# Optimization experiments

Measured on AMD Instinct MI355X. Metric: run time of the kernel, lower is better.

## Reference

```python
import jax, jax.numpy as jnp
import numpy as np

B, S = 4, 4096
DIM = 256
DF = 128   # dim_fourier = floor(256*0.5)
DS = 128   # dim_spline = 256 - 128
GF = 5     # fourier grid_size
GS = 5     # spline grid_size
K = 3      # spline order
P = 0.5
MIN_FREQ = 1e-6
LN_EPS = 1e-5


def _spline_grid():
    h = 2.0 / GS  # grid_range [-1, 1]
    g = np.arange(-K, GS + K + 1, dtype=np.float32) * h - 1.0
    return jnp.asarray(np.broadcast_to(g, (DS, g.shape[0])).copy())  # (DS, GS+2K+1)


def _base_freq():
    return jnp.asarray((1.0 / 10 ** np.linspace(0, 9, DF, dtype=np.float32)).reshape(DF, 1))


def b_splines(x, grid):
    # x: (N, DS); grid: (DS, GS+2K+1). Recursive de Boor B-spline basis.
    xe = x[:, :, None]
    bases = ((xe >= grid[:, :-1]) & (xe < grid[:, 1:])).astype(x.dtype)  # (N, DS, GS+2K)
    for k in range(1, K + 1):
        left = (xe - grid[:, : -(k + 1)]) / (grid[:, k:-1] - grid[:, : -(k + 1)])
        right = (grid[:, k + 1:] - xe) / (grid[:, k + 1:] - grid[:, 1:-k])
        bases = left * bases[:, :, :-1] + right * bases[:, :, 1:]
    return bases  # (N, DS, GS+K)


def setup_inputs() -> dict:
    key = jax.random.key(0)
    ks = jax.random.split(key, 8)
    timestamps = jax.random.uniform(ks[0], (B, S), dtype=jnp.float32)
    freq_theta = jnp.zeros((DF, 1), dtype=jnp.float32)
    bias_fourier = jnp.zeros((DF,), dtype=jnp.float32)
    fourier_weight = jax.random.normal(ks[1], (2, DF, DF, GF), dtype=jnp.float32) / (
        np.sqrt(DF) * np.sqrt(GF))
    w1_spline_w = jnp.asarray((1.0 / 10 ** np.linspace(0, 9, DS, dtype=np.float32)).reshape(DS, 1))
    w1_spline_b = jnp.zeros((DS,), dtype=jnp.float32)
    base_weight = jax.random.normal(ks[2], (DS, DS), dtype=jnp.float32) / np.sqrt(DS)
    spline_weight = jax.random.normal(ks[3], (DS, DS, GS + K), dtype=jnp.float32) / np.sqrt(DS * (GS + K))
    scale_weight = jnp.ones((DIM,), dtype=jnp.float32)
    ln_weight = jnp.ones((DIM,), dtype=jnp.float32)
    ln_bias = jnp.zeros((DIM,), dtype=jnp.float32)
    return {
        "timestamps": timestamps,
        "freq_theta": freq_theta,
        "bias_fourier": bias_fourier,
        "fourier_weight": fourier_weight,
        "w1_spline_w": w1_spline_w,
        "w1_spline_b": w1_spline_b,
        "base_weight": base_weight,
        "spline_weight": spline_weight,
        "scale_weight": scale_weight,
        "ln_weight": ln_weight,
        "ln_bias": ln_bias,
    }


def reference(timestamps, freq_theta, bias_fourier, fourier_weight,
              w1_spline_w, w1_spline_b, base_weight, spline_weight,
              scale_weight, ln_weight, ln_bias):
    grid = _spline_grid()
    base_freq = _base_freq()
    t = timestamps[..., None]  # (B, S, 1)

    # ---- Fourier branch ----
    freq_scale = jax.nn.softplus(freq_theta) + MIN_FREQ          # (DF, 1)
    freq_weight = base_freq * freq_scale                          # (DF, 1)
    proj_f = t * freq_weight[:, 0] + bias_fourier                 # (B, S, DF)
    xf = proj_f.reshape(-1, DF)                                   # (N, DF)
    kfreq = jnp.arange(1, GF + 1, dtype=xf.dtype)                 # (GF,)
    arg = xf[:, :, None] * kfreq                                  # (N, DF, GF)
    # Same math as torch's broadcast-then-sum, expressed as a contraction:
    # y[n,o] = sum_{d,g} cos(arg)[n,d,g] * Wc[o,d,g] + sin * Ws
    y_f = (jnp.einsum('ndg,odg->no', jnp.cos(arg), fourier_weight[0])
           + jnp.einsum('ndg,odg->no', jnp.sin(arg), fourier_weight[1])
           + fourier_weight[0].dtype.type(0) + jnp.zeros((DF,), xf.dtype))
    y_f = y_f  # bias of FourierSeries is zeros param; include explicitly below
    fourier_bias = jnp.zeros((DF,), xf.dtype)
    y_f = y_f + fourier_bias
    out_fourier = y_f.reshape(B, S, DF)

    # ---- Spline branch ----
    proj_s = t * w1_spline_w[:, 0] + w1_spline_b                  # (B, S, DS)
    xs = proj_s.reshape(-1, DS)                                   # (N, DS)
    base_out = jnp.tanh(xs) @ base_weight.T                       # (N, DS)
    bsp = b_splines(xs, grid).reshape(xs.shape[0], -1)            # (N, DS*(GS+K))
    spline_out = bsp @ spline_weight.reshape(DS, -1).T            # (N, DS)
    out_spline = (base_out + spline_out).reshape(B, S, DS)

    # ---- Combine (padded concat == concat of weighted halves) ----
    out = jnp.concatenate([out_fourier * P, out_spline * (1.0 - P)], axis=-1)  # (B, S, DIM)

    # LayerNorm then learnable scale
    mu = jnp.mean(out, axis=-1, keepdims=True)
    var = jnp.mean((out - mu) ** 2, axis=-1, keepdims=True)
    out = (out - mu) * jax.lax.rsqrt(var + LN_EPS) * ln_weight + ln_bias
    out = out * scale_weight
    return out
```

## Files before the change

### kernel.cpp

```cpp
#include <hip/hip_runtime.h>


typedef __attribute__((ext_vector_type(8))) _Float16 half8;
typedef __attribute__((ext_vector_type(2))) __fp16 fp16x2;
typedef __attribute__((ext_vector_type(4))) float f32x4;

#define KN5 -0.19999998807907104f
#define KN6  0.20000004768371582f
#define KN7  0.60000002384185791f

__device__ __forceinline__ unsigned pk(float a, float b) {
    fp16x2 h = __builtin_amdgcn_cvt_pkrtz(a, b);
    return __builtin_bit_cast(unsigned, h);
}

#define SPL9(x, o0,o1,o2,o3,o4,o5,o6,o7,o8) do {                          \
    float ax_ = fabsf(x);                                                  \
    float e_  = __expf(-2.f*ax_);                                          \
    float th_ = (1.f - e_) * __builtin_amdgcn_rcpf(1.f + e_);              \
    o0 = ((x) < 0.f) ? -th_ : th_;                                         \
    bool b1_ = ((x) >= KN6), b2_ = ((x) >= KN7);                           \
    float kn_ = b2_ ? KN7 : (b1_ ? KN6 : KN5);                             \
    float u_  = ((x) - kn_) * 2.5f;                                        \
    float um_ = 1.f - u_;                                                  \
    float u2_ = u_*u_, u3_ = u2_*u_, um2_ = um_*um_, um3_ = um2_*um_;      \
    float w0_ = (1.f/6.f)*um3_, w3_ = (1.f/6.f)*u3_;                       \
    float w1_ = 0.6666666666666667f - u2_  + 0.5f*u3_;                     \
    float w2_ = 0.6666666666666667f - um2_ + 0.5f*um3_;                    \
    o1 = 0.f; o2 = 0.f;                                                    \
    o3 = b1_ ? 0.f : w0_;                                                  \
    o4 = b2_ ? 0.f : (b1_ ? w0_ : w1_);                                    \
    o5 = b2_ ? w0_ : (b1_ ? w1_ : w2_);                                    \
    o6 = b2_ ? w1_ : (b1_ ? w2_ : w3_);                                    \
    o7 = b2_ ? w2_ : (b1_ ? w3_ : 0.f);                                    \
    o8 = b2_ ? w3_ : 0.f;                                                  \
} while (0)

__global__ __launch_bounds__(256) void prep_kernel(
    const float* __restrict__ FW,
    const float* __restrict__ BW,
    const float* __restrict__ SW,
    _Float16* __restrict__ WFP, _Float16* __restrict__ WSP)
{
    int tt = blockIdx.x * 256 + threadIdx.x;
    if (tt < 163840) {
        float val = FW[tt];
        int g = tt % 5;
        int r1 = tt / 5;
        int d = r1 & 127;
        int r2 = r1 >> 7;
        int col = r2 & 127;
        int p = r2 >> 7;
        int k = d*10 + p*5 + g;
        int idx = (((col>>4)*40 + (k>>5))*64 + ((k>>3)&3)*16 + (col&15))*8 + (k&7);
        WFP[idx] = (_Float16)val;
    } else if (tt < 180224) {
        int s = tt - 163840;
        float val = BW[s];
        int col = s >> 7, d = s & 127;
        int k = d*9;
        int idx = (((col>>4)*36 + (k>>5))*64 + ((k>>3)&3)*16 + (col&15))*8 + (k&7);
        WSP[idx] = (_Float16)val;
    } else if (tt < 311296) {
        int s = tt - 180224;
        float val = SW[s];
        int m = s & 7, d = (s>>3) & 127, col = s >> 10;
        int k = d*9 + m + 1;
        int idx = (((col>>4)*36 + (k>>5))*64 + ((k>>3)&3)*16 + (col&15))*8 + (k&7);
        WSP[idx] = (_Float16)val;
    }
}

__global__ __launch_bounds__(512) void fused_kernel(
    const float* __restrict__ TS, const float* __restrict__ FTHETA,
    const float* __restrict__ BFOUR, const float* __restrict__ W1W,
    const float* __restrict__ W1B, const float* __restrict__ LNW,
    const float* __restrict__ LNB, const float* __restrict__ SCW,
    const _Float16* __restrict__ WFP, const _Float16* __restrict__ WSP,
    float* __restrict__ OUT)
{
    __shared__ __align__(128) _Float16 feat0[64 * 288];
    __shared__ __align__(128) _Float16 feat1[64 * 288];
    __shared__ float tsS[64], fwS[128], bfS[128], w1wS[128], w1bS[128];
    __shared__ float redS[64][4], redQ[64][4], muS[64], rsS[64];

    const int tid  = threadIdx.x;
    const int lane = tid & 63;
    const int w    = tid >> 6;
    const int wr   = w >> 2, wc = w & 3;
    const int la15 = lane & 15, lhi = lane >> 4;
    const int row0 = blockIdx.x * 64;

    if (tid < 64) tsS[tid] = TS[row0 + tid];
    else if (tid < 192) {
        int d = tid - 64;
        float th = FTHETA[d];
        float sp = (th > 20.f) ? th : log1pf(__expf(th));
        float ex = (float)((double)d * (9.0 / 127.0));
        fwS[d] = (1.0f / powf(10.f, ex)) * (sp + 1e-6f);
        bfS[d] = BFOUR[d];
    } else if (tid < 320) {
        int d = tid - 192;
        w1wS[d] = W1W[d];
        w1bS[d] = W1B[d];
    }
    __syncthreads();

    f32x4 acc1[2][2] = {};
    f32x4 acc2[2][2] = {};

    auto computeFour = [&](int ch, _Float16* buf) {
#pragma unroll
        for (int q = 0; q < 2; ++q) {
            int task = q * 512 + tid;
            int row = task >> 4, dd = task & 15;
            int d = (ch << 4) + dd;
            float base = tsS[row] * fwS[d] + bfS[d];
            float s1, c1;
            __sincosf(base, &s1, &c1);
            float tc = c1 + c1;
            float c2 = tc*c1 - 1.f, c3 = tc*c2 - c1, c4 = tc*c3 - c2, c5 = tc*c4 - c3;
            float s2 = tc*s1,       s3 = tc*s2 - s1, s4 = tc*s3 - s2, s5 = tc*s4 - s3;
            char* p = (char*)buf;
            int b = row * 576 + dd * 20;
            int sw = (row & 7) << 4;
            *(unsigned*)(p + ((b +  0) ^ sw)) = pk(c1, c2);
            *(unsigned*)(p + ((b +  4) ^ sw)) = pk(c3, c4);
            *(unsigned*)(p + ((b +  8) ^ sw)) = pk(c5, s1);
            *(unsigned*)(p + ((b + 12) ^ sw)) = pk(s2, s3);
            *(unsigned*)(p + ((b + 16) ^ sw)) = pk(s4, s5);
        }
    };

    auto computeSpl = [&](int ch, _Float16* buf) {
#pragma unroll
        for (int q = 0; q < 2; ++q) {
            int task = q * 512 + tid;
            int row = task >> 4, dp = task & 15;
            float t = tsS[row];
            int d0 = (ch << 5) + dp * 2;
            float x0 = t * w1wS[d0]     + w1bS[d0];
            float x1 = t * w1wS[d0 + 1] + w1bS[d0 + 1];
            float a0,a1,a2,a3,a4,a5,a6,a7,a8;
            float b0,b1,b2,b3,b4,b5,b6,b7,b8;
            SPL9(x0, a0,a1,a2,a3,a4,a5,a6,a7,a8);
            SPL9(x1, b0,b1,b2,b3,b4,b5,b6,b7,b8);
            char* p = (char*)buf;
            int b = row * 576 + dp * 36;
            int sw = (row & 7) << 4;
            *(unsigned*)(p + ((b +  0) ^ sw)) = pk(a0, a1);
            *(unsigned*)(p + ((b +  4) ^ sw)) = pk(a2, a3);
            *(unsigned*)(p + ((b +  8) ^ sw)) = pk(a4, a5);
            *(unsigned*)(p + ((b + 12) ^ sw)) = pk(a6, a7);
            *(unsigned*)(p + ((b + 16) ^ sw)) = pk(a8, b0);
            *(unsigned*)(p + ((b + 20) ^ sw)) = pk(b1, b2);
            *(unsigned*)(p + ((b + 24) ^ sw)) = pk(b3, b4);
            *(unsigned*)(p + ((b + 28) ^ sw)) = pk(b5, b6);
            *(unsigned*)(p + ((b + 32) ^ sw)) = pk(b7, b8);
        }
    };

    auto mfmaFour = [&](int ch, const _Float16* buf) {
        const char* p = (const char*)buf;
#pragma unroll
        for (int kt = 0; kt < 5; ++kt) {
            int ktg = ch * 5 + kt;
            half8 bf0 = *(const half8*)(WFP + (size_t)(((wc*2 + 0)*40 + ktg)*64 + lane) * 8);
            half8 bf1 = *(const half8*)(WFP + (size_t)(((wc*2 + 1)*40 + ktg)*64 + lane) * 8);
#pragma unroll
            for (int rt = 0; rt < 2; ++rt) {
                int row = wr*32 + rt*16 + la15;
                half8 a = *(const half8*)(p + ((row*576 + kt*64 + lhi*16) ^ ((row & 7) << 4)));
                acc1[rt][0] = __builtin_amdgcn_mfma_f32_16x16x32_f16(a, bf0, acc1[rt][0], 0, 0, 0);
                acc1[rt][1] = __builtin_amdgcn_mfma_f32_16x16x32_f16(a, bf1, acc1[rt][1], 0, 0, 0);
            }
        }
    };

    auto mfmaSpl = [&](int ch, const _Float16* buf) {
        const char* p = (const char*)buf;
#pragma unroll
        for (int kt = 0; kt < 9; ++kt) {
            int ktg = ch * 9 + kt;
            half8 bf0 = *(const half8*)(WSP + (size_t)(((wc*2 + 0)*36 + ktg)*64 + lane) * 8);
            half8 bf1 = *(const half8*)(WSP + (size_t)(((wc*2 + 1)*36 + ktg)*64 + lane) * 8);
#pragma unroll
            for (int rt = 0; rt < 2; ++rt) {
                int row = wr*32 + rt*16 + la15;
                half8 a = *(const half8*)(p + ((row*576 + kt*64 + lhi*16) ^ ((row & 7) << 4)));
                acc2[rt][0] = __builtin_amdgcn_mfma_f32_16x16x32_f16(a, bf0, acc2[rt][0], 0, 0, 0);
                acc2[rt][1] = __builtin_amdgcn_mfma_f32_16x16x32_f16(a, bf1, acc2[rt][1], 0, 0, 0);
            }
        }
    };

    computeFour(0, feat0);
    __syncthreads();
    for (int ph = 0; ph < 12; ++ph) {
        _Float16* nb = ((ph + 1) & 1) ? feat1 : feat0;
        const _Float16* cb = (ph & 1) ? feat1 : feat0;
        int nx = ph + 1;
        if (nx < 8)        computeFour(nx, nb);
        else if (nx < 12)  computeSpl(nx - 8, nb);
        if (ph < 8) mfmaFour(ph, cb);
        else        mfmaSpl(ph - 8, cb);
        __syncthreads();
    }

#pragma unroll
    for (int rt = 0; rt < 2; ++rt) {
#pragma unroll
        for (int j = 0; j < 4; ++j) {
            float x0 = 0.5f * acc1[rt][0][j];
            float x1 = 0.5f * acc1[rt][1][j];
            float x2 = 0.5f * acc2[rt][0][j];
            float x3 = 0.5f * acc2[rt][1][j];
            float s  = x0 + x1 + x2 + x3;
            float qq = x0*x0 + x1*x1 + x2*x2 + x3*x3;
#pragma unroll
            for (int m = 1; m < 16; m <<= 1) {
                s  += __shfl_xor(s, m);
                qq += __shfl_xor(qq, m);
            }
            if (la15 == 0) {
                int r = wr*32 + rt*16 + lhi*4 + j;
                redS[r][wc] = s;
                redQ[r][wc] = qq;
            }
        }
    }
    __syncthreads();
    if (tid < 64) {
        float s = redS[tid][0] + redS[tid][1] + redS[tid][2] + redS[tid][3];
        float qq = redQ[tid][0] + redQ[tid][1] + redQ[tid][2] + redQ[tid][3];
        float mu = s * (1.0f / 256.0f);
        float var = qq * (1.0f / 256.0f) - mu * mu;
        muS[tid] = mu;
        rsS[tid] = rsqrtf(var + 1e-5f);
    }
    __syncthreads();
    {
        int c10 = wc*32 + la15, c11 = c10 + 16;
        int c20 = c10 + 128,    c21 = c11 + 128;
        float g10 = LNW[c10]*SCW[c10], h10 = LNB[c10]*SCW[c10];
        float g11 = LNW[c11]*SCW[c11], h11 = LNB[c11]*SCW[c11];
        float g20 = LNW[c20]*SCW[c20], h20 = LNB[c20]*SCW[c20];
        float g21 = LNW[c21]*SCW[c21], h21 = LNB[c21]*SCW[c21];
#pragma unroll
        for (int rt = 0; rt < 2; ++rt) {
#pragma unroll
            for (int j = 0; j < 4; ++j) {
                int r = wr*32 + rt*16 + lhi*4 + j;
                float mu = muS[r], rr = rsS[r];
                size_t base = (size_t)(row0 + r) * 256;
                OUT[base + c10] = (0.5f*acc1[rt][0][j] - mu)*rr*g10 + h10;
                OUT[base + c11] = (0.5f*acc1[rt][1][j] - mu)*rr*g11 + h11;
                OUT[base + c20] = (0.5f*acc2[rt][0][j] - mu)*rr*g20 + h20;
                OUT[base + c21] = (0.5f*acc2[rt][1][j] - mu)*rr*g21 + h21;
            }
        }
    }
}

extern "C" void kernel_launch(void* const* d_in, const int* in_sizes, int n_in,
                              void* d_out, int out_size, void* d_ws, size_t ws_size,
                              hipStream_t stream) {
    const float* TS     = (const float*)d_in[0];
    const float* FTHETA = (const float*)d_in[1];
    const float* BFOUR  = (const float*)d_in[2];
    const float* FW     = (const float*)d_in[3];
    const float* W1W    = (const float*)d_in[4];
    const float* W1B    = (const float*)d_in[5];
    const float* BW     = (const float*)d_in[6];
    const float* SW     = (const float*)d_in[7];
    const float* SCW    = (const float*)d_in[8];
    const float* LNW    = (const float*)d_in[9];
    const float* LNB    = (const float*)d_in[10];
    float* OUT = (float*)d_out;

    _Float16* WFP = (_Float16*)d_ws;
    _Float16* WSP = WFP + 163840;

    hipLaunchKernelGGL(prep_kernel, dim3(1216), dim3(256), 0, stream,
                       FW, BW, SW, WFP, WSP);
    hipLaunchKernelGGL(fused_kernel, dim3(256), dim3(512), 0, stream,
                       TS, FTHETA, BFOUR, W1W, W1B, LNW, LNB, SCW, WFP, WSP, OUT);
}
```

Baseline: 111.7 us.

## Switch to 32x32x16 MFMA tiles with K padded to ten per dim

Replaces the 16x16x32 f16 MFMA tiling (2x2 tiles per wave) with a single 32x32x16 MFMA tile per branch per wave. The spline K dimension is padded from 9 to 10 per input dim so both branches share a uniform 16-dim chunk layout, and the prep kernel is rewritten to emit weights in the new fragment order. Feature tiles in LDS shrink and per-thread indexing is hoisted out of the loops. The cost is about 11% more spline MMA work from the zero padding and more pipeline phases (16 instead of 12), each needing a block barrier.

```diff
diff --git a/kernel.cpp b/kernel.cpp
--- a/kernel.cpp
+++ b/kernel.cpp
@@ -3,7 +3,7 @@
 
 typedef __attribute__((ext_vector_type(8))) _Float16 half8;
 typedef __attribute__((ext_vector_type(2))) __fp16 fp16x2;
-typedef __attribute__((ext_vector_type(4))) float f32x4;
+typedef __attribute__((ext_vector_type(16))) float f32x16;
 
 #define KN5 -0.19999998807907104f
 #define KN6  0.20000004768371582f
@@ -43,32 +43,22 @@
     _Float16* __restrict__ WFP, _Float16* __restrict__ WSP)
 {
     int tt = blockIdx.x * 256 + threadIdx.x;
-    if (tt < 163840) {
-        float val = FW[tt];
-        int g = tt % 5;
-        int r1 = tt / 5;
-        int d = r1 & 127;
-        int r2 = r1 >> 7;
-        int col = r2 & 127;
-        int p = r2 >> 7;
-        int k = d*10 + p*5 + g;
-        int idx = (((col>>4)*40 + (k>>5))*64 + ((k>>3)&3)*16 + (col&15))*8 + (k&7);
-        WFP[idx] = (_Float16)val;
-    } else if (tt < 180224) {
-        int s = tt - 163840;
-        float val = BW[s];
-        int col = s >> 7, d = s & 127;
-        int k = d*9;
-        int idx = (((col>>4)*36 + (k>>5))*64 + ((k>>3)&3)*16 + (col&15))*8 + (k&7);
-        WSP[idx] = (_Float16)val;
-    } else if (tt < 311296) {
-        int s = tt - 180224;
-        float val = SW[s];
-        int m = s & 7, d = (s>>3) & 127, col = s >> 10;
-        int k = d*9 + m + 1;
-        int idx = (((col>>4)*36 + (k>>5))*64 + ((k>>3)&3)*16 + (col&15))*8 + (k&7);
-        WSP[idx] = (_Float16)val;
-    }
+    if (tt >= 327680) return;
+    int e = tt & 7, l = (tt >> 3) & 63, frag = tt >> 9;
+    int isS = frag >= 320;
+    int f = isS ? frag - 320 : frag;
+    int col = (f / 80) * 32 + (l & 31);
+    int k = (f % 80) * 16 + (l >> 5) * 8 + e;
+    int d = k / 10, j = k - d * 10;
+    float val;
+    if (!isS) {
+        int p = (j >= 5), g = j - p * 5;
+        val = FW[p * 81920 + col * 640 + d * 5 + g];
+    } else {
+        val = (j == 0) ? BW[col * 128 + d]
+            : (j <= 8) ? SW[col * 1024 + d * 8 + (j - 1)] : 0.f;
+    }
+    (isS ? WSP : WFP)[(size_t)(f * 64 + l) * 8 + e] = (_Float16)val;
 }
 
 __global__ __launch_bounds__(512) void fused_kernel(
@@ -79,8 +69,8 @@
     const _Float16* __restrict__ WFP, const _Float16* __restrict__ WSP,
     float* __restrict__ OUT)
 {
-    __shared__ __align__(128) _Float16 feat0[64 * 288];
-    __shared__ __align__(128) _Float16 feat1[64 * 288];
+    __shared__ __align__(16) _Float16 feat0[64 * 160];
+    __shared__ __align__(16) _Float16 feat1[64 * 160];
     __shared__ float tsS[64], fwS[128], bfS[128], w1wS[128], w1bS[128];
     __shared__ float redS[64][4], redQ[64][4], muS[64], rsS[64];
 
@@ -88,7 +78,7 @@
     const int lane = tid & 63;
     const int w    = tid >> 6;
     const int wr   = w >> 2, wc = w & 3;
-    const int la15 = lane & 15, lhi = lane >> 4;
+    const int l31  = lane & 31, lh = lane >> 5;
     const int row0 = blockIdx.x * 64;
 
     if (tid < 64) tsS[tid] = TS[row0 + tid];
@@ -106,24 +96,30 @@
     }
     __syncthreads();
 
-    f32x4 acc1[2][2] = {};
-    f32x4 acc2[2][2] = {};
+    const int dd   = tid & 15;
+    const int rowA = tid >> 4, rowB = rowA + 32;
+    const float tA = tsS[rowA], tB = tsS[rowB];
+    const int bA = rowA * 320 + dd * 20, swA = (rowA & 7) << 4;
+    const int bB = rowB * 320 + dd * 20, swB = (rowB & 7) << 4;
+    const int arow = wr * 32 + l31;
+    const int abase = arow * 320, aswz = (arow & 7) << 4;
+
+    f32x16 acc1 = {};
+    f32x16 acc2 = {};
 
     auto computeFour = [&](int ch, _Float16* buf) {
+        int d = ch * 16 + dd;
+        float fw = fwS[d], bf = bfS[d];
+        char* p = (char*)buf;
 #pragma unroll
         for (int q = 0; q < 2; ++q) {
-            int task = q * 512 + tid;
-            int row = task >> 4, dd = task & 15;
-            int d = (ch << 4) + dd;
-            float base = tsS[row] * fwS[d] + bfS[d];
+            float base = (q ? tB : tA) * fw + bf;
+            int b = q ? bB : bA, sw = q ? swB : swA;
             float s1, c1;
             __sincosf(base, &s1, &c1);
             float tc = c1 + c1;
             float c2 = tc*c1 - 1.f, c3 = tc*c2 - c1, c4 = tc*c3 - c2, c5 = tc*c4 - c3;
             float s2 = tc*s1,       s3 = tc*s2 - s1, s4 = tc*s3 - s2, s5 = tc*s4 - s3;
-            char* p = (char*)buf;
-            int b = row * 576 + dd * 20;
-            int sw = (row & 7) << 4;
             *(unsigned*)(p + ((b +  0) ^ sw)) = pk(c1, c2);
             *(unsigned*)(p + ((b +  4) ^ sw)) = pk(c3, c4);
             *(unsigned*)(p + ((b +  8) ^ sw)) = pk(c5, s1);
@@ -133,105 +129,76 @@
     };
 
     auto computeSpl = [&](int ch, _Float16* buf) {
+        int d = ch * 16 + dd;
+        float ww = w1wS[d], wb = w1bS[d];
+        char* p = (char*)buf;
 #pragma unroll
         for (int q = 0; q < 2; ++q) {
-            int task = q * 512 + tid;
-            int row = task >> 4, dp = task & 15;
-            float t = tsS[row];
-            int d0 = (ch << 5) + dp * 2;
-            float x0 = t * w1wS[d0]     + w1bS[d0];
-            float x1 = t * w1wS[d0 + 1] + w1bS[d0 + 1];
-            float a0,a1,a2,a3,a4,a5,a6,a7,a8;
-            float b0,b1,b2,b3,b4,b5,b6,b7,b8;
-            SPL9(x0, a0,a1,a2,a3,a4,a5,a6,a7,a8);
-            SPL9(x1, b0,b1,b2,b3,b4,b5,b6,b7,b8);
-            char* p = (char*)buf;
-            int b = row * 576 + dp * 36;
-            int sw = (row & 7) << 4;
-            *(unsigned*)(p + ((b +  0) ^ sw)) = pk(a0, a1);
-            *(unsigned*)(p + ((b +  4) ^ sw)) = pk(a2, a3);
-            *(unsigned*)(p + ((b +  8) ^ sw)) = pk(a4, a5);
-            *(unsigned*)(p + ((b + 12) ^ sw)) = pk(a6, a7);
-            *(unsigned*)(p + ((b + 16) ^ sw)) = pk(a8, b0);
-            *(unsigned*)(p + ((b + 20) ^ sw)) = pk(b1, b2);
-            *(unsigned*)(p + ((b + 24) ^ sw)) = pk(b3, b4);
-            *(unsigned*)(p + ((b + 28) ^ sw)) = pk(b5, b6);
-            *(unsigned*)(p + ((b + 32) ^ sw)) = pk(b7, b8);
-        }
-    };
-
-    auto mfmaFour = [&](int ch, const _Float16* buf) {
+            float x = (q ? tB : tA) * ww + wb;
+            int b = q ? bB : bA, sw = q ? swB : swA;
+            float t0,b0,b1,b2,b3,b4,b5,b6,b7;
+            SPL9(x, t0,b0,b1,b2,b3,b4,b5,b6,b7);
+            *(unsigned*)(p + ((b +  0) ^ sw)) = pk(t0, b0);
+            *(unsigned*)(p + ((b +  4) ^ sw)) = pk(b1, b2);
+            *(unsigned*)(p + ((b +  8) ^ sw)) = pk(b3, b4);
+            *(unsigned*)(p + ((b + 12) ^ sw)) = pk(b5, b6);
+            *(unsigned*)(p + ((b + 16) ^ sw)) = pk(b7, 0.f);
+        }
+    };
+
+    auto mfmaF = [&](int ch, const _Float16* buf) {
         const char* p = (const char*)buf;
 #pragma unroll
-        for (int kt = 0; kt < 5; ++kt) {
-            int ktg = ch * 5 + kt;
-            half8 bf0 = *(const half8*)(WFP + (size_t)(((wc*2 + 0)*40 + ktg)*64 + lane) * 8);
-            half8 bf1 = *(const half8*)(WFP + (size_t)(((wc*2 + 1)*40 + ktg)*64 + lane) * 8);
-#pragma unroll
-            for (int rt = 0; rt < 2; ++rt) {
-                int row = wr*32 + rt*16 + la15;
-                half8 a = *(const half8*)(p + ((row*576 + kt*64 + lhi*16) ^ ((row & 7) << 4)));
-                acc1[rt][0] = __builtin_amdgcn_mfma_f32_16x16x32_f16(a, bf0, acc1[rt][0], 0, 0, 0);
-                acc1[rt][1] = __builtin_amdgcn_mfma_f32_16x16x32_f16(a, bf1, acc1[rt][1], 0, 0, 0);
-            }
-        }
-    };
-
-    auto mfmaSpl = [&](int ch, const _Float16* buf) {
+        for (int ks = 0; ks < 10; ++ks) {
+            half8 b = *(const half8*)(WFP + (size_t)((wc*80 + ch*10 + ks)*64 + lane) * 8);
+            half8 a = *(const half8*)(p + ((abase + ks*32 + lh*16) ^ aswz));
+            acc1 = __builtin_amdgcn_mfma_f32_32x32x16_f16(a, b, acc1, 0, 0, 0);
+        }
+    };
+
+    auto mfmaS = [&](int ch, const _Float16* buf) {
         const char* p = (const char*)buf;
 #pragma unroll
-        for (int kt = 0; kt < 9; ++kt) {
-            int ktg = ch * 9 + kt;
-            half8 bf0 = *(const half8*)(WSP + (size_t)(((wc*2 + 0)*36 + ktg)*64 + lane) * 8);
-            half8 bf1 = *(const half8*)(WSP + (size_t)(((wc*2 + 1)*36 + ktg)*64 + lane) * 8);
-#pragma unroll
-            for (int rt = 0; rt < 2; ++rt) {
-                int row = wr*32 + rt*16 + la15;
-                half8 a = *(const half8*)(p + ((row*576 + kt*64 + lhi*16) ^ ((row & 7) << 4)));
-                acc2[rt][0] = __builtin_amdgcn_mfma_f32_16x16x32_f16(a, bf0, acc2[rt][0], 0, 0, 0);
-                acc2[rt][1] = __builtin_amdgcn_mfma_f32_16x16x32_f16(a, bf1, acc2[rt][1], 0, 0, 0);
-            }
+        for (int ks = 0; ks < 10; ++ks) {
+            half8 b = *(const half8*)(WSP + (size_t)((wc*80 + ch*10 + ks)*64 + lane) * 8);
+            half8 a = *(const half8*)(p + ((abase + ks*32 + lh*16) ^ aswz));
+            acc2 = __builtin_amdgcn_mfma_f32_32x32x16_f16(a, b, acc2, 0, 0, 0);
         }
     };
 
     computeFour(0, feat0);
     __syncthreads();
-    for (int ph = 0; ph < 12; ++ph) {
+    for (int ph = 0; ph < 16; ++ph) {
         _Float16* nb = ((ph + 1) & 1) ? feat1 : feat0;
         const _Float16* cb = (ph & 1) ? feat1 : feat0;
         int nx = ph + 1;
-        if (nx < 8)        computeFour(nx, nb);
-        else if (nx < 12)  computeSpl(nx - 8, nb);
-        if (ph < 8) mfmaFour(ph, cb);
-        else        mfmaSpl(ph - 8, cb);
+        if (nx < 8)       computeFour(nx, nb);
+        else if (nx < 16) computeSpl(nx - 8, nb);
+        if (ph < 8) mfmaF(ph, cb);
+        else        mfmaS(ph - 8, cb);
         __syncthreads();
     }
 
 #pragma unroll
-    for (int rt = 0; rt < 2; ++rt) {
-#pragma unroll
-        for (int j = 0; j < 4; ++j) {
-            float x0 = 0.5f * acc1[rt][0][j];
-            float x1 = 0.5f * acc1[rt][1][j];
-            float x2 = 0.5f * acc2[rt][0][j];
-            float x3 = 0.5f * acc2[rt][1][j];
-            float s  = x0 + x1 + x2 + x3;
-            float qq = x0*x0 + x1*x1 + x2*x2 + x3*x3;
-#pragma unroll
-            for (int m = 1; m < 16; m <<= 1) {
-                s  += __shfl_xor(s, m);
-                qq += __shfl_xor(qq, m);
-            }
-            if (la15 == 0) {
-                int r = wr*32 + rt*16 + lhi*4 + j;
-                redS[r][wc] = s;
-                redQ[r][wc] = qq;
-            }
+    for (int g = 0; g < 16; ++g) {
+        float xf = 0.5f * acc1[g];
+        float xs = 0.5f * acc2[g];
+        float s  = xf + xs;
+        float qq = xf*xf + xs*xs;
+#pragma unroll
+        for (int m = 1; m < 32; m <<= 1) {
+            s  += __shfl_xor(s, m);
+            qq += __shfl_xor(qq, m);
+        }
+        if (l31 == 0) {
+            int r = wr*32 + (g & 3) + 8*(g >> 2) + 4*lh;
+            redS[r][wc] = s;
+            redQ[r][wc] = qq;
         }
     }
     __syncthreads();
     if (tid < 64) {
-        float s = redS[tid][0] + redS[tid][1] + redS[tid][2] + redS[tid][3];
+        float s  = redS[tid][0] + redS[tid][1] + redS[tid][2] + redS[tid][3];
         float qq = redQ[tid][0] + redQ[tid][1] + redQ[tid][2] + redQ[tid][3];
         float mu = s * (1.0f / 256.0f);
         float var = qq * (1.0f / 256.0f) - mu * mu;
@@ -240,24 +207,16 @@
     }
     __syncthreads();
     {
-        int c10 = wc*32 + la15, c11 = c10 + 16;
-        int c20 = c10 + 128,    c21 = c11 + 128;
-        float g10 = LNW[c10]*SCW[c10], h10 = LNB[c10]*SCW[c10];
-        float g11 = LNW[c11]*SCW[c11], h11 = LNB[c11]*SCW[c11];
-        float g20 = LNW[c20]*SCW[c20], h20 = LNB[c20]*SCW[c20];
-        float g21 = LNW[c21]*SCW[c21], h21 = LNB[c21]*SCW[c21];
-#pragma unroll
-        for (int rt = 0; rt < 2; ++rt) {
-#pragma unroll
-            for (int j = 0; j < 4; ++j) {
-                int r = wr*32 + rt*16 + lhi*4 + j;
-                float mu = muS[r], rr = rsS[r];
-                size_t base = (size_t)(row0 + r) * 256;
-                OUT[base + c10] = (0.5f*acc1[rt][0][j] - mu)*rr*g10 + h10;
-                OUT[base + c11] = (0.5f*acc1[rt][1][j] - mu)*rr*g11 + h11;
-                OUT[base + c20] = (0.5f*acc2[rt][0][j] - mu)*rr*g20 + h20;
-                OUT[base + c21] = (0.5f*acc2[rt][1][j] - mu)*rr*g21 + h21;
-            }
+        int cF = wc*32 + l31, cS = cF + 128;
+        float gF = LNW[cF]*SCW[cF], hF = LNB[cF]*SCW[cF];
+        float gS = LNW[cS]*SCW[cS], hS = LNB[cS]*SCW[cS];
+#pragma unroll
+        for (int g = 0; g < 16; ++g) {
+            int r = wr*32 + (g & 3) + 8*(g >> 2) + 4*lh;
+            float mu = muS[r], rr = rsS[r];
+            size_t base = (size_t)(row0 + r) * 256;
+            OUT[base + cF] = (0.5f*acc1[g] - mu)*rr*gF + hF;
+            OUT[base + cS] = (0.5f*acc2[g] - mu)*rr*gS + hS;
         }
     }
 }
@@ -281,7 +240,7 @@
     _Float16* WFP = (_Float16*)d_ws;
     _Float16* WSP = WFP + 163840;
 
-    hipLaunchKernelGGL(prep_kernel, dim3(1216), dim3(256), 0, stream,
+    hipLaunchKernelGGL(prep_kernel, dim3(1280), dim3(256), 0, stream,
                        FW, BW, SW, WFP, WSP);
     hipLaunchKernelGGL(fused_kernel, dim3(256), dim3(512), 0, stream,
                        TS, FTHETA, BFOUR, W1W, W1B, LNW, LNB, SCW, WFP, WSP, OUT);
```

After: 113.8 us. About the same (+1.8%).
